# Performance work log

Hardware: AMD Instinct MI355X
Metric: run time of the kernel (lower is better)

## Reference

```python
import jax, jax.numpy as jnp
import numpy as np

B, S, HID, H = 4, 1024, 1024, 16
D = HID // H


def setup_inputs() -> dict:
    key = jax.random.key(0)
    ks = jax.random.split(key, 4)
    scale = 0.02
    return {
        "hidden_states": jax.random.normal(ks[0], (B, S, HID), dtype=jnp.float32),
        "attention_mask": jnp.ones((B, S), dtype=jnp.int32),
        "layer_head_mask": jnp.ones((H,), dtype=jnp.float32),
        "Wq": jax.random.normal(ks[1], (HID, HID), dtype=jnp.float32) * scale,
        "bq": jnp.zeros((HID,), dtype=jnp.float32),
        "Wk": jax.random.normal(ks[2], (HID, HID), dtype=jnp.float32) * scale,
        "bk": jnp.zeros((HID,), dtype=jnp.float32),
        "Wv": jax.random.normal(ks[3], (HID, HID), dtype=jnp.float32) * scale,
        "bv": jnp.zeros((HID,), dtype=jnp.float32),
    }


def reference(hidden_states, attention_mask, layer_head_mask, Wq, bq, Wk, bk, Wv, bv):
    b, s, _ = hidden_states.shape
    # QKV projections, split heads: [B,S,H,D]
    q = (hidden_states @ Wq + bq).reshape(b, s, H, D)
    k = (hidden_states @ Wk + bk).reshape(b, s, H, D)
    v = (hidden_states @ Wv + bv).reshape(b, s, H, D)

    # attention bias from padding mask: [B,1,1,S]
    mask = attention_mask[:, None, None, :]
    neg = jnp.finfo(jnp.float32).min
    bias = jnp.where(mask > 0, 0.0, neg).astype(jnp.float32)

    # dot_product_attention_weights: scale query by 1/sqrt(D)
    q = q / jnp.sqrt(jnp.asarray(D, dtype=q.dtype))
    scores = jnp.einsum("bqhd,bkhd->bhqk", q, k) + bias  # [B,H,S,S]
    attn_weights = jax.nn.softmax(scores, axis=-1)

    # per-head masking
    attn_weights = attn_weights * layer_head_mask[None, :, None, None]

    attn_output = jnp.einsum("bhqk,bkhd->bqhd", attn_weights, v)
    return attn_output.reshape(b, s, HID)
```

## Files before the change

### kernel.cpp

```cpp
#include <hip/hip_runtime.h>
#include <stdint.h>

typedef __bf16 bf16_t;
typedef bf16_t __attribute__((ext_vector_type(8))) bf16x8;
typedef float __attribute__((ext_vector_type(4))) f32x4;
typedef float __attribute__((ext_vector_type(16))) f32x16;
typedef unsigned u32;

#define BATCH 4
#define SEQ 1024
#define HIDD 1024
#define NH 16
#define DH 64

__device__ __forceinline__ unsigned short f2bf(float f) {
  unsigned u = __float_as_uint(f);
  u += 0x7fffu + ((u >> 16) & 1u);
  return (unsigned short)(u >> 16);
}

__device__ __forceinline__ f32x4 mfma16(bf16x8 a, bf16x8 b, f32x4 c) {
  return __builtin_amdgcn_mfma_f32_16x16x32_bf16(a, b, c, 0, 0, 0);
}
__device__ __forceinline__ f32x16 mfma32(bf16x8 a, bf16x8 b, f32x16 c) {
  return __builtin_amdgcn_mfma_f32_32x32x16_bf16(a, b, c, 0, 0, 0);
}

__device__ __forceinline__ u32 cvtpk(float lo, float hi) {
  u32 r;
  asm("v_cvt_pk_bf16_f32 %0, %1, %2" : "=v"(r) : "v"(lo), "v"(hi));
  return r;
}
__device__ __forceinline__ void plswap(u32& a, u32& b) {
  asm("v_permlane32_swap_b32 %0, %1" : "+v"(a), "+v"(b));
}

__global__ __launch_bounds__(256) void prep(
    const float* __restrict__ hs, unsigned short* __restrict__ Apack,
    const float* __restrict__ Wq, const float* __restrict__ Wk,
    const float* __restrict__ Wv, unsigned short* __restrict__ Bpack) {
  __shared__ unsigned short tile[64][72];
  const int bid = blockIdx.x;
  const int t = threadIdx.x;
  if (bid < 4096) {
    const float4 f = ((const float4*)hs)[bid * 256 + t];
    ushort4 o = make_ushort4(f2bf(f.x), f2bf(f.y), f2bf(f.z), f2bf(f.w));
    const int mt = bid >> 4, lc = bid & 15;
    const int kt = t >> 3, lg = (t >> 1) & 3, e = (t & 1) * 4;
    *(ushort4*)(Apack + (size_t)mt * 16384 + kt * 512 + (lg * 16 + lc) * 8 + e) = o;
    return;
  }
  const int id = bid - 4096;
  const int z = id >> 8, rem = id & 255;
  const int k0 = (rem & 15) * 64, n0 = (rem >> 4) * 64;
  const float* W = (z == 0) ? Wq : (z == 1) ? Wk : Wv;
  unsigned short* o = Bpack + (size_t)z * (1024 * 1024);
  const int r = t >> 6, c = t & 63;
#pragma unroll
  for (int i = 0; i < 16; ++i) {
    const int row = i * 4 + r;
    tile[row][c] = f2bf(W[(size_t)(k0 + row) * 1024 + n0 + c]);
  }
  __syncthreads();
  const int q = t >> 6, l = t & 63, lc = l & 15, lg = l >> 4;
#pragma unroll
  for (int it = 0; it < 2; ++it) {
    const int nt = (rem >> 4) * 4 + q;
    const int kt = (rem & 15) * 2 + it;
    unsigned short buf[8];
#pragma unroll
    for (int e = 0; e < 8; ++e)
      buf[e] = tile[it * 32 + lg * 8 + e][q * 16 + lc];
    *(uint4*)(o + (size_t)nt * 16384 + kt * 512 + l * 8) = *(uint4*)buf;
  }
}

__global__ __launch_bounds__(256, 3) void qkv_gemm(
    const unsigned short* __restrict__ Apack,
    const unsigned short* __restrict__ Bpack,
    const float* __restrict__ bq, const float* __restrict__ bk,
    const float* __restrict__ bv,
    unsigned short* __restrict__ Qb,
    unsigned short* __restrict__ Kpk,
    unsigned short* __restrict__ Vpk) {
  const int id = blockIdx.x;
  const int j = id >> 3;
  const int mx = (id & 7) * 4 + (j & 3);
  const int rest = j >> 2;
  const int nx = rest & 7;
  const int z = rest >> 3;

  const float* bias = (z == 0) ? bq : (z == 1) ? bk : bv;
  const float scale = (z == 0) ? 0.125f * 1.44269504089f : 1.0f;
  const int m0 = mx * 128, n0 = nx * 128;
  const int t = threadIdx.x;
  const int w = t >> 6, l = t & 63;
  const int lg = l >> 4, lc = l & 15;
  const int wr = w >> 1, wc = w & 1;

  const unsigned short* Ap = Apack + (size_t)(mx * 8 + wr * 4) * 16384 + l * 8;
  const unsigned short* Bp = Bpack + (size_t)z * (1024 * 1024) +
                             (size_t)(nx * 8 + wc * 4) * 16384 + l * 8;

  f32x4 acc[4][4] = {};
  bf16x8 a0[4], b0[4], a1[4], b1[4];

#pragma unroll
  for (int m = 0; m < 4; ++m) {
    a0[m] = *(const bf16x8*)(Ap + m * 16384);
    b0[m] = *(const bf16x8*)(Bp + m * 16384);
  }

  for (int kk = 0; kk < 16; ++kk) {
    const int kt = kk * 2;
#pragma unroll
    for (int m = 0; m < 4; ++m) {
      a1[m] = *(const bf16x8*)(Ap + m * 16384 + (kt + 1) * 512);
      b1[m] = *(const bf16x8*)(Bp + m * 16384 + (kt + 1) * 512);
    }
#pragma unroll
    for (int m = 0; m < 4; ++m)
#pragma unroll
      for (int n = 0; n < 4; ++n)
        acc[m][n] = mfma16(a0[m], b0[n], acc[m][n]);
    if (kk < 15) {
#pragma unroll
      for (int m = 0; m < 4; ++m) {
        a0[m] = *(const bf16x8*)(Ap + m * 16384 + (kt + 2) * 512);
        b0[m] = *(const bf16x8*)(Bp + m * 16384 + (kt + 2) * 512);
      }
    }
#pragma unroll
    for (int m = 0; m < 4; ++m)
#pragma unroll
      for (int n = 0; n < 4; ++n)
        acc[m][n] = mfma16(a1[m], b1[n], acc[m][n]);
  }

  if (z == 0) {
#pragma unroll
    for (int n = 0; n < 4; ++n) {
      const int col = n0 + wc * 64 + n * 16 + lc;
      const float bs = bias[col];
#pragma unroll
      for (int m = 0; m < 4; ++m)
#pragma unroll
        for (int r = 0; r < 4; ++r) {
          const int row = m0 + wr * 64 + m * 16 + lg * 4 + r;
          Qb[(size_t)row * 1024 + col] = f2bf((acc[m][n][r] + bs) * scale);
        }
    }
  } else if (z == 1) {
#pragma unroll
    for (int n = 0; n < 4; ++n) {
      const int col = n0 + wc * 64 + n * 16 + lc;
      const float bs = bias[col];
      const int h = col >> 6, s = (col >> 4) & 3, hi = (col >> 3) & 1, e = col & 7;
#pragma unroll
      for (int m = 0; m < 4; ++m)
#pragma unroll
        for (int r = 0; r < 4; ++r) {
          const int row = m0 + wr * 64 + m * 16 + lg * 4 + r;
          const int bh = (row >> 10) * 16 + h, tl = row & 1023;
          const int kb = tl >> 5, lo = tl & 31;
          Kpk[(size_t)(((bh * 32 + kb) * 4 + s) * 512) + (lo + hi * 32) * 8 + e] =
              f2bf(acc[m][n][r] + bs);
        }
    }
  } else {
#pragma unroll
    for (int n = 0; n < 4; ++n) {
      const int col = n0 + wc * 64 + n * 16 + lc;
      const float bs = bias[col];
      const int h = col >> 6, g = (col >> 5) & 1, lo = col & 31;
#pragma unroll
      for (int m = 0; m < 4; ++m)
#pragma unroll
        for (int r = 0; r < 4; ++r) {
          const int row = m0 + wr * 64 + m * 16 + lg * 4 + r;
          const int bh = (row >> 10) * 16 + h, tl = row & 1023;
          const int kt = tl >> 6, within = tl & 63;
          const int sv = within >> 4, hiv = (within >> 3) & 1, ev = within & 7;
          Vpk[(size_t)(((bh * 16 + kt) * 8 + g * 4 + sv) * 512) +
              (lo + hiv * 32) * 8 + ev] = f2bf(acc[m][n][r] + bs);
        }
    }
  }
}

__global__ __launch_bounds__(256, 2) void attn_kernel(
    const unsigned short* __restrict__ Qb,
    const unsigned short* __restrict__ Kpack,
    const unsigned short* __restrict__ Vpack,
    const int* __restrict__ amask,
    const float* __restrict__ lhm,
    float* __restrict__ out) {
  const int id = blockIdx.x;
  const int swzid = (id & 7) * 64 + (id >> 3);
  const int qt = swzid & 7;
  const int bh = swzid >> 3;
  const int b = bh >> 4, h = bh & 15;
  const int t = threadIdx.x;
  const int w = t >> 6, l = t & 63;
  const int lo = l & 31, hi = l >> 5;
  const int q0 = qt * 128 + w * 32;

  const unsigned short* Kp = Kpack + (size_t)bh * 65536 + l * 8;
  const unsigned short* Vp = Vpack + (size_t)bh * 65536 + l * 8;

  const unsigned short* qp = Qb + (size_t)(b * SEQ + q0 + lo) * HIDD + h * DH + hi * 8;
  bf16x8 qf[4];
#pragma unroll
  for (int s = 0; s < 4; ++s) qf[s] = *(const bf16x8*)(qp + s * 16);

  bool needmask;
  {
    unsigned long long mm = ~0ull;
#pragma unroll
    for (int tk = 0; tk < 16; ++tk)
      mm &= __ballot(amask[b * SEQ + tk * 64 + l] > 0);
    needmask = (mm != ~0ull);
  }

  float m_run = -INFINITY, l_run = 0.f;
  f32x16 acc0 = {}, acc1 = {};

  bf16x8 kf0[4], kf1[4], vf0[4], vf1[4];

#pragma unroll
  for (int s = 0; s < 4; ++s) {
    kf0[s] = *(const bf16x8*)(Kp + (s)*512);
    kf1[s] = *(const bf16x8*)(Kp + (4 + s) * 512);
  }

  for (int tk = 0; tk < 16; ++tk) {
#pragma unroll
    for (int s = 0; s < 4; ++s) {
      vf0[s] = *(const bf16x8*)(Vp + (size_t)(tk * 8 + s) * 512);
      vf1[s] = *(const bf16x8*)(Vp + (size_t)(tk * 8 + 4 + s) * 512);
    }

    f32x16 sg0 = {}, sg1 = {};
    __builtin_amdgcn_s_setprio(1);
#pragma unroll
    for (int s = 0; s < 4; ++s) {
      sg0 = mfma32(kf0[s], qf[s], sg0);
      sg1 = mfma32(kf1[s], qf[s], sg1);
    }
    __builtin_amdgcn_s_setprio(0);

    if (tk < 15) {
#pragma unroll
      for (int s = 0; s < 4; ++s) {
        kf0[s] = *(const bf16x8*)(Kp + (size_t)(tk * 8 + 8 + s) * 512);
        kf1[s] = *(const bf16x8*)(Kp + (size_t)(tk * 8 + 12 + s) * 512);
      }
    }

    float t0[8];
#pragma unroll
    for (int i = 0; i < 8; ++i)
      t0[i] = fmaxf(fmaxf(sg0[i], sg0[i + 8]), fmaxf(sg1[i], sg1[i + 8]));
    float t1 = fmaxf(fmaxf(fmaxf(t0[0], t0[1]), fmaxf(t0[2], t0[3])),
                     fmaxf(fmaxf(t0[4], t0[5]), fmaxf(t0[6], t0[7])));
    const float pmax = fmaxf(t1, __shfl_xor(t1, 32));

    if (!__all(pmax <= m_run + 8.f)) {
      const float mnew = fmaxf(m_run, pmax);
      const float sc = __builtin_amdgcn_exp2f(m_run - mnew);
      m_run = mnew;
      l_run *= sc;
#pragma unroll
      for (int g = 0; g < 16; ++g) {
        const int rowi = (g & 3) + 8 * (g >> 2) + 4 * hi;
        const float scr = __shfl(sc, rowi);
        acc0[g] *= scr;
        acc1[g] *= scr;
      }
    }

#pragma unroll
    for (int g = 0; g < 16; ++g) {
      sg0[g] = __builtin_amdgcn_exp2f(sg0[g] - m_run);
      sg1[g] = __builtin_amdgcn_exp2f(sg1[g] - m_run);
    }

    if (needmask) {
      const int mv = amask[b * SEQ + tk * 64 + l];
      const unsigned long long m64 = __ballot(mv > 0);
      if (m64 != ~0ull) {
#pragma unroll
        for (int g = 0; g < 16; ++g) {
          const int krow = (g & 3) + 8 * (g >> 2) + 4 * hi;
          if (!((m64 >> krow) & 1)) sg0[g] = 0.f;
          if (!((m64 >> (krow + 32)) & 1)) sg1[g] = 0.f;
        }
      }
    }

    float s0[8];
#pragma unroll
    for (int i = 0; i < 8; ++i)
      s0[i] = (sg0[i] + sg0[i + 8]) + (sg1[i] + sg1[i + 8]);
    float rs = ((s0[0] + s0[1]) + (s0[2] + s0[3])) +
               ((s0[4] + s0[5]) + (s0[6] + s0[7]));
    rs += __shfl_xor(rs, 32);
    l_run += rs;

    auto mk = [](float a0, float a1, float a2, float a3,
                 float a4, float a5, float a6, float a7) -> bf16x8 {
      u32 x = cvtpk(a0, a1), y = cvtpk(a2, a3);
      u32 a = cvtpk(a4, a5), b2 = cvtpk(a6, a7);
      plswap(x, a);
      plswap(y, b2);
      union { u32 u[4]; bf16x8 v; } fu;
      fu.u[0] = x; fu.u[1] = y; fu.u[2] = a; fu.u[3] = b2;
      return fu.v;
    };
    const bf16x8 pa0 = mk(sg0[0], sg0[1], sg0[2], sg0[3], sg0[4], sg0[5], sg0[6], sg0[7]);
    const bf16x8 pa1 = mk(sg0[8], sg0[9], sg0[10], sg0[11], sg0[12], sg0[13], sg0[14], sg0[15]);
    const bf16x8 pa2 = mk(sg1[0], sg1[1], sg1[2], sg1[3], sg1[4], sg1[5], sg1[6], sg1[7]);
    const bf16x8 pa3 = mk(sg1[8], sg1[9], sg1[10], sg1[11], sg1[12], sg1[13], sg1[14], sg1[15]);

    __builtin_amdgcn_s_setprio(1);
#pragma unroll
    for (int s = 0; s < 4; ++s) {
      const bf16x8 paf = (s == 0) ? pa0 : (s == 1) ? pa1 : (s == 2) ? pa2 : pa3;
      acc0 = mfma32(paf, vf0[s], acc0);
      acc1 = mfma32(paf, vf1[s], acc1);
    }
    __builtin_amdgcn_s_setprio(0);
  }

  const float hm = lhm[h];
  const float inv = hm / l_run;
  float* ob = out + (size_t)(b * SEQ + q0) * HIDD + h * DH + lo;
#pragma unroll
  for (int g = 0; g < 16; ++g) {
    const int rowi = (g & 3) + 8 * (g >> 2) + 4 * hi;
    const float iv = __shfl(inv, rowi);
    ob[(size_t)rowi * HIDD] = acc0[g] * iv;
    ob[(size_t)rowi * HIDD + 32] = acc1[g] * iv;
  }
}

extern "C" void kernel_launch(void* const* d_in, const int* in_sizes, int n_in,
                              void* d_out, int out_size, void* d_ws, size_t ws_size,
                              hipStream_t stream) {
  const float* hs = (const float*)d_in[0];
  const int* amask = (const int*)d_in[1];
  const float* lhm = (const float*)d_in[2];
  const float* Wq = (const float*)d_in[3];
  const float* bq = (const float*)d_in[4];
  const float* Wk = (const float*)d_in[5];
  const float* bk = (const float*)d_in[6];
  const float* Wv = (const float*)d_in[7];
  const float* bv = (const float*)d_in[8];
  float* out = (float*)d_out;

  char* ws = (char*)d_ws;
  unsigned short* Apack = (unsigned short*)ws;
  unsigned short* Bpack = (unsigned short*)(ws + (8u << 20));
  unsigned short* Qb = (unsigned short*)(ws + (14u << 20));
  unsigned short* Kpk = (unsigned short*)(ws + (22u << 20));
  unsigned short* Vpk = (unsigned short*)(ws + (30u << 20));

  prep<<<4864, 256, 0, stream>>>(hs, Apack, Wq, Wk, Wv, Bpack);
  qkv_gemm<<<768, 256, 0, stream>>>(Apack, Bpack, bq, bk, bv, Qb, Kpk, Vpk);
  attn_kernel<<<512, 256, 0, stream>>>(Qb, Kpk, Vpk, amask, lhm, out);
}
```

Baseline: 79.32 us.

## Process two query tiles per wave to reuse K/V fragments

After: 86.05 us. +8.5%, slower.

```diff
diff --git a/kernel.cpp b/kernel.cpp
--- a/kernel.cpp
+++ b/kernel.cpp
@@ -188,7 +188,7 @@
   }
 }
 
-__global__ __launch_bounds__(256, 2) void attn_kernel(
+__global__ __launch_bounds__(256, 1) void attn_kernel(
     const unsigned short* __restrict__ Qb,
     const unsigned short* __restrict__ Kpack,
     const unsigned short* __restrict__ Vpack,
@@ -196,22 +196,27 @@
     const float* __restrict__ lhm,
     float* __restrict__ out) {
   const int id = blockIdx.x;
-  const int swzid = (id & 7) * 64 + (id >> 3);
-  const int qt = swzid & 7;
-  const int bh = swzid >> 3;
+  const int swzid = (id & 7) * 32 + (id >> 3);
+  const int qt = swzid & 3;
+  const int bh = swzid >> 2;
   const int b = bh >> 4, h = bh & 15;
   const int t = threadIdx.x;
   const int w = t >> 6, l = t & 63;
   const int lo = l & 31, hi = l >> 5;
-  const int q0 = qt * 128 + w * 32;
+  const int q0a = qt * 256 + w * 32;
+  const int q0b = q0a + 128;
 
   const unsigned short* Kp = Kpack + (size_t)bh * 65536 + l * 8;
   const unsigned short* Vp = Vpack + (size_t)bh * 65536 + l * 8;
 
-  const unsigned short* qp = Qb + (size_t)(b * SEQ + q0 + lo) * HIDD + h * DH + hi * 8;
-  bf16x8 qf[4];
-#pragma unroll
-  for (int s = 0; s < 4; ++s) qf[s] = *(const bf16x8*)(qp + s * 16);
+  const unsigned short* qpa = Qb + (size_t)(b * SEQ + q0a + lo) * HIDD + h * DH + hi * 8;
+  const unsigned short* qpb = Qb + (size_t)(b * SEQ + q0b + lo) * HIDD + h * DH + hi * 8;
+  bf16x8 qa[4], qb2[4];
+#pragma unroll
+  for (int s = 0; s < 4; ++s) {
+    qa[s] = *(const bf16x8*)(qpa + s * 16);
+    qb2[s] = *(const bf16x8*)(qpb + s * 16);
+  }
 
   bool needmask;
   {
@@ -222,8 +227,8 @@
     needmask = (mm != ~0ull);
   }
 
-  float m_run = -INFINITY, l_run = 0.f;
-  f32x16 acc0 = {}, acc1 = {};
+  float mA = -INFINITY, lA = 0.f, mB = -INFINITY, lB = 0.f;
+  f32x16 accA0 = {}, accA1 = {}, accB0 = {}, accB1 = {};
 
   bf16x8 kf0[4], kf1[4], vf0[4], vf1[4];
 
@@ -233,6 +238,17 @@
     kf1[s] = *(const bf16x8*)(Kp + (4 + s) * 512);
   }
 
+  auto mk = [](float a0, float a1, float a2, float a3,
+               float a4, float a5, float a6, float a7) -> bf16x8 {
+    u32 x = cvtpk(a0, a1), y = cvtpk(a2, a3);
+    u32 a = cvtpk(a4, a5), b2 = cvtpk(a6, a7);
+    plswap(x, a);
+    plswap(y, b2);
+    union { u32 u[4]; bf16x8 v; } fu;
+    fu.u[0] = x; fu.u[1] = y; fu.u[2] = a; fu.u[3] = b2;
+    return fu.v;
+  };
+
   for (int tk = 0; tk < 16; ++tk) {
 #pragma unroll
     for (int s = 0; s < 4; ++s) {
@@ -240,12 +256,17 @@
       vf1[s] = *(const bf16x8*)(Vp + (size_t)(tk * 8 + 4 + s) * 512);
     }
 
-    f32x16 sg0 = {}, sg1 = {};
+    f32x16 sA0 = {}, sA1 = {}, sB0 = {}, sB1 = {};
     __builtin_amdgcn_s_setprio(1);
 #pragma unroll
     for (int s = 0; s < 4; ++s) {
-      sg0 = mfma32(kf0[s], qf[s], sg0);
-      sg1 = mfma32(kf1[s], qf[s], sg1);
+      sA0 = mfma32(kf0[s], qa[s], sA0);
+      sA1 = mfma32(kf1[s], qa[s], sA1);
+    }
+#pragma unroll
+    for (int s = 0; s < 4; ++s) {
+      sB0 = mfma32(kf0[s], qb2[s], sB0);
+      sB1 = mfma32(kf1[s], qb2[s], sB1);
     }
     __builtin_amdgcn_s_setprio(0);
 
@@ -257,90 +278,151 @@
       }
     }
 
-    float t0[8];
-#pragma unroll
-    for (int i = 0; i < 8; ++i)
-      t0[i] = fmaxf(fmaxf(sg0[i], sg0[i + 8]), fmaxf(sg1[i], sg1[i + 8]));
-    float t1 = fmaxf(fmaxf(fmaxf(t0[0], t0[1]), fmaxf(t0[2], t0[3])),
-                     fmaxf(fmaxf(t0[4], t0[5]), fmaxf(t0[6], t0[7])));
-    const float pmax = fmaxf(t1, __shfl_xor(t1, 32));
-
-    if (!__all(pmax <= m_run + 8.f)) {
-      const float mnew = fmaxf(m_run, pmax);
-      const float sc = __builtin_amdgcn_exp2f(m_run - mnew);
-      m_run = mnew;
-      l_run *= sc;
-#pragma unroll
-      for (int g = 0; g < 16; ++g) {
-        const int rowi = (g & 3) + 8 * (g >> 2) + 4 * hi;
-        const float scr = __shfl(sc, rowi);
-        acc0[g] *= scr;
-        acc1[g] *= scr;
-      }
-    }
-
-#pragma unroll
-    for (int g = 0; g < 16; ++g) {
-      sg0[g] = __builtin_amdgcn_exp2f(sg0[g] - m_run);
-      sg1[g] = __builtin_amdgcn_exp2f(sg1[g] - m_run);
-    }
-
+    unsigned long long m64 = ~0ull;
+    bool tilemask = false;
     if (needmask) {
       const int mv = amask[b * SEQ + tk * 64 + l];
-      const unsigned long long m64 = __ballot(mv > 0);
-      if (m64 != ~0ull) {
+      m64 = __ballot(mv > 0);
+      tilemask = (m64 != ~0ull);
+    }
+
+    {
+      float t0[8];
+#pragma unroll
+      for (int i = 0; i < 8; ++i)
+        t0[i] = fmaxf(fmaxf(sA0[i], sA0[i + 8]), fmaxf(sA1[i], sA1[i + 8]));
+      float t1 = fmaxf(fmaxf(fmaxf(t0[0], t0[1]), fmaxf(t0[2], t0[3])),
+                       fmaxf(fmaxf(t0[4], t0[5]), fmaxf(t0[6], t0[7])));
+      const float pmax = fmaxf(t1, __shfl_xor(t1, 32));
+      if (!__all(pmax <= mA + 8.f)) {
+        const float mnew = fmaxf(mA, pmax);
+        const float sc = __builtin_amdgcn_exp2f(mA - mnew);
+        mA = mnew;
+        lA *= sc;
+#pragma unroll
+        for (int g = 0; g < 16; ++g) {
+          const int rowi = (g & 3) + 8 * (g >> 2) + 4 * hi;
+          const float scr = __shfl(sc, rowi);
+          accA0[g] *= scr;
+          accA1[g] *= scr;
+        }
+      }
+#pragma unroll
+      for (int g = 0; g < 16; ++g) {
+        sA0[g] = __builtin_amdgcn_exp2f(sA0[g] - mA);
+        sA1[g] = __builtin_amdgcn_exp2f(sA1[g] - mA);
+      }
+      if (tilemask) {
 #pragma unroll
         for (int g = 0; g < 16; ++g) {
           const int krow = (g & 3) + 8 * (g >> 2) + 4 * hi;
-          if (!((m64 >> krow) & 1)) sg0[g] = 0.f;
-          if (!((m64 >> (krow + 32)) & 1)) sg1[g] = 0.f;
-        }
-      }
-    }
-
-    float s0[8];
-#pragma unroll
-    for (int i = 0; i < 8; ++i)
-      s0[i] = (sg0[i] + sg0[i + 8]) + (sg1[i] + sg1[i + 8]);
-    float rs = ((s0[0] + s0[1]) + (s0[2] + s0[3])) +
-               ((s0[4] + s0[5]) + (s0[6] + s0[7]));
-    rs += __shfl_xor(rs, 32);
-    l_run += rs;
-
-    auto mk = [](float a0, float a1, float a2, float a3,
-                 float a4, float a5, float a6, float a7) -> bf16x8 {
-      u32 x = cvtpk(a0, a1), y = cvtpk(a2, a3);
-      u32 a = cvtpk(a4, a5), b2 = cvtpk(a6, a7);
-      plswap(x, a);
-      plswap(y, b2);
-      union { u32 u[4]; bf16x8 v; } fu;
-      fu.u[0] = x; fu.u[1] = y; fu.u[2] = a; fu.u[3] = b2;
-      return fu.v;
-    };
-    const bf16x8 pa0 = mk(sg0[0], sg0[1], sg0[2], sg0[3], sg0[4], sg0[5], sg0[6], sg0[7]);
-    const bf16x8 pa1 = mk(sg0[8], sg0[9], sg0[10], sg0[11], sg0[12], sg0[13], sg0[14], sg0[15]);
-    const bf16x8 pa2 = mk(sg1[0], sg1[1], sg1[2], sg1[3], sg1[4], sg1[5], sg1[6], sg1[7]);
-    const bf16x8 pa3 = mk(sg1[8], sg1[9], sg1[10], sg1[11], sg1[12], sg1[13], sg1[14], sg1[15]);
-
-    __builtin_amdgcn_s_setprio(1);
-#pragma unroll
-    for (int s = 0; s < 4; ++s) {
-      const bf16x8 paf = (s == 0) ? pa0 : (s == 1) ? pa1 : (s == 2) ? pa2 : pa3;
-      acc0 = mfma32(paf, vf0[s], acc0);
-      acc1 = mfma32(paf, vf1[s], acc1);
-    }
-    __builtin_amdgcn_s_setprio(0);
+          if (!((m64 >> krow) & 1)) sA0[g] = 0.f;
+          if (!((m64 >> (krow + 32)) & 1)) sA1[g] = 0.f;
+        }
+      }
+      float s0[8];
+#pragma unroll
+      for (int i = 0; i < 8; ++i)
+        s0[i] = (sA0[i] + sA0[i + 8]) + (sA1[i] + sA1[i + 8]);
+      float rs = ((s0[0] + s0[1]) + (s0[2] + s0[3])) +
+                 ((s0[4] + s0[5]) + (s0[6] + s0[7]));
+      rs += __shfl_xor(rs, 32);
+      lA += rs;
+
+      const bf16x8 p0 = mk(sA0[0], sA0[1], sA0[2], sA0[3], sA0[4], sA0[5], sA0[6], sA0[7]);
+      const bf16x8 p1 = mk(sA0[8], sA0[9], sA0[10], sA0[11], sA0[12], sA0[13], sA0[14], sA0[15]);
+      const bf16x8 p2 = mk(sA1[0], sA1[1], sA1[2], sA1[3], sA1[4], sA1[5], sA1[6], sA1[7]);
+      const bf16x8 p3 = mk(sA1[8], sA1[9], sA1[10], sA1[11], sA1[12], sA1[13], sA1[14], sA1[15]);
+      __builtin_amdgcn_s_setprio(1);
+#pragma unroll
+      for (int s = 0; s < 4; ++s) {
+        const bf16x8 paf = (s == 0) ? p0 : (s == 1) ? p1 : (s == 2) ? p2 : p3;
+        accA0 = mfma32(paf, vf0[s], accA0);
+        accA1 = mfma32(paf, vf1[s], accA1);
+      }
+      __builtin_amdgcn_s_setprio(0);
+    }
+
+    {
+      float t0[8];
+#pragma unroll
+      for (int i = 0; i < 8; ++i)
+        t0[i] = fmaxf(fmaxf(sB0[i], sB0[i + 8]), fmaxf(sB1[i], sB1[i + 8]));
+      float t1 = fmaxf(fmaxf(fmaxf(t0[0], t0[1]), fmaxf(t0[2], t0[3])),
+                       fmaxf(fmaxf(t0[4], t0[5]), fmaxf(t0[6], t0[7])));
+      const float pmax = fmaxf(t1, __shfl_xor(t1, 32));
+      if (!__all(pmax <= mB + 8.f)) {
+        const float mnew = fmaxf(mB, pmax);
+        const float sc = __builtin_amdgcn_exp2f(mB - mnew);
+        mB = mnew;
+        lB *= sc;
+#pragma unroll
+        for (int g = 0; g < 16; ++g) {
+          const int rowi = (g & 3) + 8 * (g >> 2) + 4 * hi;
+          const float scr = __shfl(sc, rowi);
+          accB0[g] *= scr;
+          accB1[g] *= scr;
+        }
+      }
+#pragma unroll
+      for (int g = 0; g < 16; ++g) {
+        sB0[g] = __builtin_amdgcn_exp2f(sB0[g] - mB);
+        sB1[g] = __builtin_amdgcn_exp2f(sB1[g] - mB);
+      }
+      if (tilemask) {
+#pragma unroll
+        for (int g = 0; g < 16; ++g) {
+          const int krow = (g & 3) + 8 * (g >> 2) + 4 * hi;
+          if (!((m64 >> krow) & 1)) sB0[g] = 0.f;
+          if (!((m64 >> (krow + 32)) & 1)) sB1[g] = 0.f;
+        }
+      }
+      float s0[8];
+#pragma unroll
+      for (int i = 0; i < 8; ++i)
+        s0[i] = (sB0[i] + sB0[i + 8]) + (sB1[i] + sB1[i + 8]);
+      float rs = ((s0[0] + s0[1]) + (s0[2] + s0[3])) +
+                 ((s0[4] + s0[5]) + (s0[6] + s0[7]));
+      rs += __shfl_xor(rs, 32);
+      lB += rs;
+
+      const bf16x8 p0 = mk(sB0[0], sB0[1], sB0[2], sB0[3], sB0[4], sB0[5], sB0[6], sB0[7]);
+      const bf16x8 p1 = mk(sB0[8], sB0[9], sB0[10], sB0[11], sB0[12], sB0[13], sB0[14], sB0[15]);
+      const bf16x8 p2 = mk(sB1[0], sB1[1], sB1[2], sB1[3], sB1[4], sB1[5], sB1[6], sB1[7]);
+      const bf16x8 p3 = mk(sB1[8], sB1[9], sB1[10], sB1[11], sB1[12], sB1[13], sB1[14], sB1[15]);
+      __builtin_amdgcn_s_setprio(1);
+#pragma unroll
+      for (int s = 0; s < 4; ++s) {
+        const bf16x8 paf = (s == 0) ? p0 : (s == 1) ? p1 : (s == 2) ? p2 : p3;
+        accB0 = mfma32(paf, vf0[s], accB0);
+        accB1 = mfma32(paf, vf1[s], accB1);
+      }
+      __builtin_amdgcn_s_setprio(0);
+    }
   }
 
   const float hm = lhm[h];
-  const float inv = hm / l_run;
-  float* ob = out + (size_t)(b * SEQ + q0) * HIDD + h * DH + lo;
-#pragma unroll
-  for (int g = 0; g < 16; ++g) {
-    const int rowi = (g & 3) + 8 * (g >> 2) + 4 * hi;
-    const float iv = __shfl(inv, rowi);
-    ob[(size_t)rowi * HIDD] = acc0[g] * iv;
-    ob[(size_t)rowi * HIDD + 32] = acc1[g] * iv;
+  {
+    const float inv = hm / lA;
+    float* ob = out + (size_t)(b * SEQ + q0a) * HIDD + h * DH + lo;
+#pragma unroll
+    for (int g = 0; g < 16; ++g) {
+      const int rowi = (g & 3) + 8 * (g >> 2) + 4 * hi;
+      const float iv = __shfl(inv, rowi);
+      ob[(size_t)rowi * HIDD] = accA0[g] * iv;
+      ob[(size_t)rowi * HIDD + 32] = accA1[g] * iv;
+    }
+  }
+  {
+    const float inv = hm / lB;
+    float* ob = out + (size_t)(b * SEQ + q0b) * HIDD + h * DH + lo;
+#pragma unroll
+    for (int g = 0; g < 16; ++g) {
+      const int rowi = (g & 3) + 8 * (g >> 2) + 4 * hi;
+      const float iv = __shfl(inv, rowi);
+      ob[(size_t)rowi * HIDD] = accB0[g] * iv;
+      ob[(size_t)rowi * HIDD + 32] = accB1[g] * iv;
+    }
   }
 }
 
@@ -367,5 +449,5 @@
 
   prep<<<4864, 256, 0, stream>>>(hs, Apack, Wq, Wk, Wv, Bpack);
   qkv_gemm<<<768, 256, 0, stream>>>(Apack, Bpack, bq, bk, bv, Qb, Kpk, Vpk);
-  attn_kernel<<<512, 256, 0, stream>>>(Qb, Kpk, Vpk, amask, lhm, out);
-}
+  attn_kernel<<<256, 256, 0, stream>>>(Qb, Kpk, Vpk, amask, lhm, out);
+}
```
